# Optimization experiments

Hardware: AMD Instinct MI355X
Metric: run time of the kernel (lower is better)

The kernel has to match this reference:

```python
import jax, jax.numpy as jnp
import numpy as np

NUM_LEVELS = 16
FEATS_PER_LEVEL = 2
LOG2_HASHMAP = 19
TABLE_SIZE = 1 << LOG2_HASHMAP
BASE_RES = 16
DESIRED_RES = 4096
PER_LEVEL_SCALE = float(np.exp(np.log(DESIRED_RES / BASE_RES) / (NUM_LEVELS - 1)))
PRIMES = (np.uint32(1), np.uint32(2654435761), np.uint32(805459861))
N_POINTS = 2_000_000


def _level_features(x, table, level):
    # x: [N,3] in [0,1]; table: [TABLE_SIZE, F]
    scale = BASE_RES * (PER_LEVEL_SCALE ** level) - 1.0
    res = int(np.ceil(scale)) + 1
    dense = (res ** 3) <= TABLE_SIZE  # tcnn uses dense indexing when grid fits
    pos = x * scale + 0.5
    pos0 = jnp.floor(pos)
    w = pos - pos0                     # trilinear weights, [N,3]
    base = pos0.astype(jnp.uint32)
    out = jnp.zeros((x.shape[0], table.shape[1]), dtype=table.dtype)
    for c in range(8):                 # 8 corners of the voxel
        offs = [(c >> d) & 1 for d in range(3)]
        pc = [jnp.minimum(base[:, d] + np.uint32(offs[d]), np.uint32(res - 1)) for d in range(3)]
        if dense:
            idx = pc[0] + pc[1] * np.uint32(res) + pc[2] * np.uint32(res * res)
        else:
            idx = (pc[0] * PRIMES[0]) ^ (pc[1] * PRIMES[1]) ^ (pc[2] * PRIMES[2])
            idx = idx & np.uint32(TABLE_SIZE - 1)
        wt = jnp.ones(x.shape[0], dtype=x.dtype)
        for d in range(3):
            wt = wt * (w[:, d] if offs[d] else (1.0 - w[:, d]))
        out = out + wt[:, None] * table[idx.astype(jnp.int32)]
    return out


def hashgrid_encode(x, tables):
    # x: [N,3] in [0,1]; tables: [L, TABLE_SIZE, F] -> [N, L*F]
    return jnp.concatenate(
        [_level_features(x, tables[l], l) for l in range(NUM_LEVELS)], axis=-1)


def setup_inputs() -> dict:
    key = jax.random.key(0)
    k1, k2, k3, k4, k5 = jax.random.split(key, 5)
    points = jax.random.uniform(k1, (N_POINTS, 3), dtype=jnp.float32)
    # tcnn hashgrid init: uniform(-1e-4, 1e-4)
    tables = jax.random.uniform(k2, (NUM_LEVELS, TABLE_SIZE, FEATS_PER_LEVEL),
                                minval=-1e-4, maxval=1e-4, dtype=jnp.float32)
    def kaiming(k, fan_out, fan_in):
        bound = np.sqrt(2.0) * np.sqrt(3.0 / fan_in)
        return jax.random.uniform(k, (fan_out, fan_in), minval=-bound, maxval=bound,
                                  dtype=jnp.float32)
    W1 = kaiming(k3, 32, 32)
    W2 = kaiming(k4, 32, 32)
    W3 = kaiming(k5, 4, 32)
    aabb = jnp.stack([jnp.zeros(3, jnp.float32), jnp.ones(3, jnp.float32)])
    return {"points": points, "tables": tables, "W1": W1, "W2": W2, "W3": W3,
            "aabb": aabb}


def reference(points, tables, W1, W2, W3, aabb):
    texc = jnp.clip((points - aabb[0][None, :]) / (aabb[1] - aabb[0])[None, :], 0.0, 1.0)
    enc = hashgrid_encode(texc, tables)            # [N, 32]
    h = jax.nn.relu(enc @ W1.T)
    h = jax.nn.relu(h @ W2.T)
    out = h @ W3.T                                 # [N, 4]
    mn = jnp.array([0.0, 0.0, 0.0, 0.01], dtype=out.dtype)
    mx = jnp.array([1.0, 1.0, 1.0, 1.0], dtype=out.dtype)
    return jax.nn.sigmoid(out) * (mx - mn) + mn
```

## Files before the change

### kernel.cpp

```cpp
#include <hip/hip_runtime.h>
#include <cmath>


namespace {
constexpr int kLevels = 16;
constexpr unsigned kTableSize = 1u << 19;
constexpr unsigned kMask = kTableSize - 1u;
constexpr int kCells = 262144;
constexpr int kScanBlocks = 256;

typedef _Float16 half2_t __attribute__((ext_vector_type(2)));
typedef unsigned int u32;

struct LevelParams {
  float scale[kLevels];
  unsigned res[kLevels];
  int dense[kLevels];
  unsigned toff[kLevels];
  unsigned cnt[kLevels];
};
}

__global__ __launch_bounds__(256)
void conv_tables_kernel(const float2* __restrict__ src, u32* __restrict__ dst,
                        LevelParams lp,
                        const float* __restrict__ W1, const float* __restrict__ W2,
                        const float* __restrict__ W3, half2_t* __restrict__ Wh,
                        u32* __restrict__ hist0)
{
  int gid = blockIdx.x * blockDim.x + threadIdx.x;
  if (gid < 512) {
    Wh[gid] = half2_t{(_Float16)W1[2 * gid], (_Float16)W1[2 * gid + 1]};
  } else if (gid < 1024) {
    int t = gid - 512;
    Wh[512 + t] = half2_t{(_Float16)W2[2 * t], (_Float16)W2[2 * t + 1]};
  } else if (gid < 1088) {
    int t = gid - 1024;
    Wh[1024 + t] = half2_t{(_Float16)W3[2 * t], (_Float16)W3[2 * t + 1]};
  }
  if (hist0 && gid < kCells) hist0[gid] = 0u;
  int l = blockIdx.x >> 11;
  unsigned e = (unsigned)((blockIdx.x & 2047) * blockDim.x + threadIdx.x);
  if (l < kLevels && e < lp.cnt[l]) {
    float2 v = src[(size_t)l * kTableSize + e];
    dst[lp.toff[l] + e] =
        __builtin_bit_cast(u32, half2_t{(_Float16)v.x, (_Float16)v.y});
  }
}

__device__ __forceinline__ void texc_of(const float* __restrict__ pts,
                                        const float* __restrict__ aabb, int i,
                                        float& x, float& y, float& z)
{
  float a0x = aabb[0], a0y = aabb[1], a0z = aabb[2];
  float a1x = aabb[3], a1y = aabb[4], a1z = aabb[5];
  x = fminf(fmaxf((pts[3 * i + 0] - a0x) / (a1x - a0x), 0.f), 1.f);
  y = fminf(fmaxf((pts[3 * i + 1] - a0y) / (a1y - a0y), 0.f), 1.f);
  z = fminf(fmaxf((pts[3 * i + 2] - a0z) / (a1z - a0z), 0.f), 1.f);
}

__device__ __forceinline__ u32 expand3(u32 v)
{
  v &= 0x3FFu;
  v = (v | (v << 16)) & 0x030000FFu;
  v = (v | (v << 8))  & 0x0300F00Fu;
  v = (v | (v << 4))  & 0x030C30C3u;
  v = (v | (v << 2))  & 0x09249249u;
  return v;
}

__device__ __forceinline__ u32 cell_of(float x, float y, float z)
{
  u32 cx = (u32)min((int)(x * 64.f), 63);
  u32 cy = (u32)min((int)(y * 64.f), 63);
  u32 cz = (u32)min((int)(z * 64.f), 63);
  return expand3(cx) | (expand3(cy) << 1) | (expand3(cz) << 2);
}

__global__ __launch_bounds__(256)
void hist_kernel(const float* __restrict__ points, const float* __restrict__ aabb,
                 u32* __restrict__ hist, int n)
{
  int i = blockIdx.x * blockDim.x + threadIdx.x;
  if (i >= n) return;
  float x, y, z;
  texc_of(points, aabb, i, x, y, z);
  atomicAdd(&hist[cell_of(x, y, z)], 1u);
}

__global__ __launch_bounds__(1024)
void scanA_kernel(u32* __restrict__ hist, u32* __restrict__ btot)
{
  __shared__ u32 sm[1024];
  int t = threadIdx.x;
  int i = (blockIdx.x << 10) + t;
  u32 x = hist[i];
  sm[t] = x;
  __syncthreads();
  u32 v = x;
  for (int off = 1; off < 1024; off <<= 1) {
    u32 a = (t >= off) ? sm[t - off] : 0u;
    __syncthreads();
    v += a;
    sm[t] = v;
    __syncthreads();
  }
  hist[i] = v - x;
  if (t == 1023) btot[blockIdx.x] = v;
}

__global__ __launch_bounds__(256)
void scatter_kernel(const float* __restrict__ points, const float* __restrict__ aabb,
                    u32* __restrict__ hist, const u32* __restrict__ btot,
                    float4* __restrict__ sorted, int n)
{
  __shared__ u32 bb[kScanBlocks];
  int t = threadIdx.x;
  u32 xv = btot[t];
  bb[t] = xv;
  __syncthreads();
  u32 v = xv;
  for (int off = 1; off < 256; off <<= 1) {
    u32 a = (t >= off) ? bb[t - off] : 0u;
    __syncthreads();
    v += a;
    bb[t] = v;
    __syncthreads();
  }
  u32 excl = v - xv;
  __syncthreads();
  bb[t] = excl;
  __syncthreads();

  int i = blockIdx.x * 256 + t;
  if (i >= n) return;
  float x, y, z;
  texc_of(points, aabb, i, x, y, z);
  u32 c = cell_of(x, y, z);
  u32 slot = bb[c >> 10] + atomicAdd(&hist[c], 1u);
  sorted[slot] = float4{x, y, z, __builtin_bit_cast(float, (u32)i)};
}

__device__ __forceinline__ u32 sel4(uint4 v, u32 j) {
  u32 lo = (j & 1u) ? v.y : v.x;
  u32 hi = (j & 1u) ? v.w : v.z;
  return (j & 2u) ? hi : lo;
}

__device__ __forceinline__ float dot2_acc(half2_t a, half2_t b, float c) {
#if __has_builtin(__builtin_amdgcn_fdot2)
  return __builtin_amdgcn_fdot2(a, b, c, false);
#else
  return c + (float)a.x * (float)b.x + (float)a.y * (float)b.y;
#endif
}

__global__ __launch_bounds__(256)
void encode_kernel(const float4* __restrict__ pts,
                   const u32* __restrict__ tables,
                   half2_t* __restrict__ enc,
                   LevelParams lp, int n, int bpl)
{
  int l = blockIdx.x / bpl;
  int i = (blockIdx.x - l * bpl) * blockDim.x + threadIdx.x;
  if (i >= n) return;

  float4 p = pts[i];
  float x = p.x, y = p.y, z = p.z;

  float s = lp.scale[l];
  unsigned res = lp.res[l];
  bool dense = (lp.dense[l] != 0);
  unsigned rm1 = res - 1u;
  unsigned res2 = res * res;
  const u32* tab = tables + lp.toff[l];

  float fx = x * s + 0.5f, fy = y * s + 0.5f, fz = z * s + 0.5f;
  float fx0 = floorf(fx), fy0 = floorf(fy), fz0 = floorf(fz);
  float wx = fx - fx0, wy = fy - fy0, wz = fz - fz0;
  unsigned bx = (unsigned)fx0, by = (unsigned)fy0, bz = (unsigned)fz0;

  unsigned pcx0 = min(bx, rm1), pcx1 = min(bx + 1u, rm1);

  u32 idx0[4], idx1[4];
  #pragma unroll
  for (int q = 0; q < 4; ++q) {
    unsigned oy = (unsigned)(q & 1);
    unsigned oz = (unsigned)(q >> 1);
    unsigned pcy = min(by + oy, rm1);
    unsigned pcz = min(bz + oz, rm1);
    if (dense) {
      u32 b = pcy * res + pcz * res2;
      idx0[q] = pcx0 + b;
      idx1[q] = pcx1 + b;
    } else {
      u32 h = (pcy * 2654435761u) ^ (pcz * 805459861u);
      idx0[q] = (pcx0 ^ h) & kMask;
      idx1[q] = (pcx1 ^ h) & kMask;
    }
  }

  uint4 v[4];
  #pragma unroll
  for (int q = 0; q < 4; ++q)
    v[q] = *reinterpret_cast<const uint4*>(tab + (idx0[q] & ~3u));

  u32 e1x[4] = {0u, 0u, 0u, 0u};
  #pragma unroll
  for (int q = 0; q < 4; ++q) {
    if ((idx0[q] ^ idx1[q]) >= 4u) e1x[q] = tab[idx1[q]];
  }

  float wx1 = wx, wx0 = 1.f - wx;
  float acc0 = 0.f, acc1 = 0.f;
  #pragma unroll
  for (int q = 0; q < 4; ++q) {
    unsigned oy = (unsigned)(q & 1);
    unsigned oz = (unsigned)(q >> 1);
    float wyz = (oy ? wy : 1.f - wy) * (oz ? wz : 1.f - wz);
    u32 e0 = sel4(v[q], idx0[q] & 3u);
    u32 e1g = sel4(v[q], idx1[q] & 3u);
    u32 e1 = ((idx0[q] ^ idx1[q]) < 4u) ? e1g : e1x[q];
    half2_t f0 = __builtin_bit_cast(half2_t, e0);
    half2_t f1 = __builtin_bit_cast(half2_t, e1);
    float w0 = wyz * wx0, w1 = wyz * wx1;
    acc0 += w0 * (float)f0.x + w1 * (float)f1.x;
    acc1 += w0 * (float)f0.y + w1 * (float)f1.y;
  }
  enc[(size_t)l * n + i] = half2_t{(_Float16)acc0, (_Float16)acc1};
}

__global__ __launch_bounds__(256)
void encode_raw_kernel(const float* __restrict__ points,
                       const u32* __restrict__ tables,
                       const float* __restrict__ aabb,
                       half2_t* __restrict__ enc,
                       LevelParams lp, int n, int bpl)
{
  int l = blockIdx.x / bpl;
  int i = (blockIdx.x - l * bpl) * blockDim.x + threadIdx.x;
  if (i >= n) return;
  float x, y, z;
  texc_of(points, aabb, i, x, y, z);

  float s = lp.scale[l];
  unsigned res = lp.res[l];
  bool dense = (lp.dense[l] != 0);
  unsigned rm1 = res - 1u;
  unsigned res2 = res * res;
  const u32* tab = tables + lp.toff[l];

  float fx = x * s + 0.5f, fy = y * s + 0.5f, fz = z * s + 0.5f;
  float fx0 = floorf(fx), fy0 = floorf(fy), fz0 = floorf(fz);
  float wx = fx - fx0, wy = fy - fy0, wz = fz - fz0;
  unsigned bx = (unsigned)fx0, by = (unsigned)fy0, bz = (unsigned)fz0;
  unsigned pcx0 = min(bx, rm1), pcx1 = min(bx + 1u, rm1);

  u32 idx0[4], idx1[4];
  #pragma unroll
  for (int q = 0; q < 4; ++q) {
    unsigned oy = (unsigned)(q & 1);
    unsigned oz = (unsigned)(q >> 1);
    unsigned pcy = min(by + oy, rm1);
    unsigned pcz = min(bz + oz, rm1);
    if (dense) {
      u32 b = pcy * res + pcz * res2;
      idx0[q] = pcx0 + b;
      idx1[q] = pcx1 + b;
    } else {
      u32 h = (pcy * 2654435761u) ^ (pcz * 805459861u);
      idx0[q] = (pcx0 ^ h) & kMask;
      idx1[q] = (pcx1 ^ h) & kMask;
    }
  }
  uint4 v[4];
  #pragma unroll
  for (int q = 0; q < 4; ++q)
    v[q] = *reinterpret_cast<const uint4*>(tab + (idx0[q] & ~3u));
  u32 e1x[4] = {0u, 0u, 0u, 0u};
  #pragma unroll
  for (int q = 0; q < 4; ++q) {
    if ((idx0[q] ^ idx1[q]) >= 4u) e1x[q] = tab[idx1[q]];
  }
  float wx1 = wx, wx0 = 1.f - wx;
  float acc0 = 0.f, acc1 = 0.f;
  #pragma unroll
  for (int q = 0; q < 4; ++q) {
    unsigned oy = (unsigned)(q & 1);
    unsigned oz = (unsigned)(q >> 1);
    float wyz = (oy ? wy : 1.f - wy) * (oz ? wz : 1.f - wz);
    u32 e0 = sel4(v[q], idx0[q] & 3u);
    u32 e1g = sel4(v[q], idx1[q] & 3u);
    u32 e1 = ((idx0[q] ^ idx1[q]) < 4u) ? e1g : e1x[q];
    half2_t f0 = __builtin_bit_cast(half2_t, e0);
    half2_t f1 = __builtin_bit_cast(half2_t, e1);
    float w0 = wyz * wx0, w1 = wyz * wx1;
    acc0 += w0 * (float)f0.x + w1 * (float)f1.x;
    acc1 += w0 * (float)f0.y + w1 * (float)f1.y;
  }
  enc[(size_t)l * n + i] = half2_t{(_Float16)acc0, (_Float16)acc1};
}

__global__ __launch_bounds__(256)
void mlp_kernel(const half2_t* __restrict__ enc,
                const half2_t* __restrict__ Wh,
                const float* __restrict__ sortedw,
                float* __restrict__ out, int n)
{
  int i = blockIdx.x * blockDim.x + threadIdx.x;
  if (i >= n) return;

  u32 orig = sortedw ? __builtin_bit_cast(u32, sortedw[4 * i + 3]) : (u32)i;

  half2_t e[16];
  #pragma unroll
  for (int l = 0; l < kLevels; ++l) e[l] = enc[(size_t)l * n + i];

  const half2_t* W1h = Wh;
  const half2_t* W2h = Wh + 512;
  const half2_t* W3h = Wh + 1024;

  half2_t h1[16];
  #pragma unroll
  for (int jj = 0; jj < 16; ++jj) {
    float a0 = 0.f, a1 = 0.f;
    #pragma unroll
    for (int k = 0; k < 16; ++k) {
      a0 = dot2_acc(e[k], W1h[16 * (2 * jj) + k], a0);
      a1 = dot2_acc(e[k], W1h[16 * (2 * jj + 1) + k], a1);
    }
    h1[jj] = half2_t{(_Float16)fmaxf(a0, 0.f), (_Float16)fmaxf(a1, 0.f)};
  }

  half2_t h2[16];
  #pragma unroll
  for (int jj = 0; jj < 16; ++jj) {
    float a0 = 0.f, a1 = 0.f;
    #pragma unroll
    for (int k = 0; k < 16; ++k) {
      a0 = dot2_acc(h1[k], W2h[16 * (2 * jj) + k], a0);
      a1 = dot2_acc(h1[k], W2h[16 * (2 * jj + 1) + k], a1);
    }
    h2[jj] = half2_t{(_Float16)fmaxf(a0, 0.f), (_Float16)fmaxf(a1, 0.f)};
  }

  float o[4];
  #pragma unroll
  for (int j = 0; j < 4; ++j) {
    float acc = 0.f;
    #pragma unroll
    for (int k = 0; k < 16; ++k) acc = dot2_acc(h2[k], W3h[16 * j + k], acc);
    o[j] = acc;
  }

  float4 r;
  r.x = 1.f / (1.f + __expf(-o[0]));
  r.y = 1.f / (1.f + __expf(-o[1]));
  r.z = 1.f / (1.f + __expf(-o[2]));
  r.w = 0.99f / (1.f + __expf(-o[3])) + 0.01f;
  reinterpret_cast<float4*>(out)[orig] = r;
}

__global__ __launch_bounds__(256)
void hashgrid_mlp_kernel(const float* __restrict__ points,
                         const float* __restrict__ tables,
                         const float* __restrict__ W1,
                         const float* __restrict__ W2,
                         const float* __restrict__ W3,
                         const float* __restrict__ aabb,
                         float* __restrict__ out,
                         LevelParams lp, int n)
{
  int i = blockIdx.x * blockDim.x + threadIdx.x;
  if (i >= n) return;
  float x, y, z;
  texc_of(points, aabb, i, x, y, z);
  float enc[2 * kLevels];
  #pragma unroll
  for (int l = 0; l < kLevels; ++l) {
    float s = lp.scale[l];
    unsigned res = lp.res[l];
    bool dense = (lp.dense[l] != 0);
    unsigned rm1 = res - 1u;
    unsigned res2 = res * res;
    float fx = x * s + 0.5f, fy = y * s + 0.5f, fz = z * s + 0.5f;
    float fx0 = floorf(fx), fy0 = floorf(fy), fz0 = floorf(fz);
    float wx = fx - fx0, wy = fy - fy0, wz = fz - fz0;
    unsigned bx = (unsigned)fx0, by = (unsigned)fy0, bz = (unsigned)fz0;
    const float2* tab = reinterpret_cast<const float2*>(tables) + (size_t)l * kTableSize;
    float acc0 = 0.f, acc1 = 0.f;
    #pragma unroll
    for (int c = 0; c < 8; ++c) {
      unsigned ox = (unsigned)(c & 1);
      unsigned oy = (unsigned)((c >> 1) & 1);
      unsigned oz = (unsigned)((c >> 2) & 1);
      unsigned pcx = min(bx + ox, rm1);
      unsigned pcy = min(by + oy, rm1);
      unsigned pcz = min(bz + oz, rm1);
      unsigned idx;
      if (dense) idx = pcx + pcy * res + pcz * res2;
      else idx = (pcx ^ (pcy * 2654435761u) ^ (pcz * 805459861u)) & kMask;
      float wt = (ox ? wx : 1.f - wx) * (oy ? wy : 1.f - wy) * (oz ? wz : 1.f - wz);
      float2 f = tab[idx];
      acc0 += wt * f.x;
      acc1 += wt * f.y;
    }
    enc[2 * l + 0] = acc0;
    enc[2 * l + 1] = acc1;
  }
  float h1[32];
  #pragma unroll
  for (int j = 0; j < 32; ++j) {
    float acc = 0.f;
    #pragma unroll
    for (int k = 0; k < 32; ++k) acc += enc[k] * W1[32 * j + k];
    h1[j] = fmaxf(acc, 0.f);
  }
  float h2[32];
  #pragma unroll
  for (int j = 0; j < 32; ++j) {
    float acc = 0.f;
    #pragma unroll
    for (int k = 0; k < 32; ++k) acc += h1[k] * W2[32 * j + k];
    h2[j] = fmaxf(acc, 0.f);
  }
  float o[4];
  #pragma unroll
  for (int j = 0; j < 4; ++j) {
    float acc = 0.f;
    #pragma unroll
    for (int k = 0; k < 32; ++k) acc += h2[k] * W3[32 * j + k];
    o[j] = acc;
  }
  float4 r;
  r.x = 1.f / (1.f + __expf(-o[0]));
  r.y = 1.f / (1.f + __expf(-o[1]));
  r.z = 1.f / (1.f + __expf(-o[2]));
  r.w = 0.99f / (1.f + __expf(-o[3])) + 0.01f;
  reinterpret_cast<float4*>(out)[i] = r;
}

extern "C" void kernel_launch(void* const* d_in, const int* in_sizes, int n_in,
                              void* d_out, int out_size, void* d_ws, size_t ws_size,
                              hipStream_t stream) {
  const float* points = (const float*)d_in[0];
  const float* tables = (const float*)d_in[1];
  const float* W1     = (const float*)d_in[2];
  const float* W2     = (const float*)d_in[3];
  const float* W3     = (const float*)d_in[4];
  const float* aabb   = (const float*)d_in[5];
  float* out = (float*)d_out;
  int n = in_sizes[0] / 3;

  LevelParams lp;
  const double pls = std::exp(std::log(4096.0 / 16.0) / 15.0);
  unsigned off = 0;
  for (int l = 0; l < kLevels; ++l) {
    double s = 16.0 * std::pow(pls, (double)l) - 1.0;
    lp.scale[l] = (float)s;
    long long res = (long long)std::ceil(s) + 1;
    lp.res[l] = (unsigned)res;
    long long r3 = res * res * res;
    lp.dense[l] = (r3 <= (long long)kTableSize) ? 1 : 0;
    lp.cnt[l] = lp.dense[l] ? (unsigned)r3 : kTableSize;
    lp.toff[l] = off;
    off += (lp.cnt[l] + 3u) & ~3u;
  }

  const int block = 256;
  const size_t tab_f16_bytes = (size_t)off * sizeof(u32);
  const size_t sorted_bytes  = (size_t)n * sizeof(float4);
  const size_t hist_bytes    = (size_t)(kCells + kScanBlocks) * sizeof(u32);
  const size_t enc_bytes     = (size_t)kLevels * (size_t)n * sizeof(half2_t);
  const size_t w_bytes       = 1088 * sizeof(half2_t);

  const size_t need_sorted = tab_f16_bytes + sorted_bytes + hist_bytes +
                             enc_bytes + w_bytes;
  const size_t need_sorted_real = tab_f16_bytes + sorted_bytes + enc_bytes + w_bytes;
  const size_t need_sorted_tight = tab_f16_bytes + enc_bytes + w_bytes +
                                   ((size_t)n * sizeof(u32));
  (void)need_sorted_tight;

  const size_t need_raw = tab_f16_bytes + enc_bytes + w_bytes;
  const bool out_fits_scratch = (size_t)out_size >= (size_t)4 * (size_t)n;

  const int grid_n = (n + block - 1) / block;
  const int bpl = grid_n;

  if (ws_size >= need_sorted_real) {
    char* p = (char*)d_ws;
    u32*     tab_f16 = (u32*)p;                   p += tab_f16_bytes;
    float4*  sorted  = (float4*)p;                p += sorted_bytes;
    half2_t* enc     = (half2_t*)p;               p += enc_bytes;
    half2_t* Wh      = (half2_t*)p;
    u32*     hist    = (u32*)enc;
    u32*     btot    = hist + kCells;

    conv_tables_kernel<<<kLevels * 2048, block, 0, stream>>>(
        reinterpret_cast<const float2*>(tables), tab_f16, lp, W1, W2, W3, Wh, hist);
    hist_kernel<<<grid_n, block, 0, stream>>>(points, aabb, hist, n);
    scanA_kernel<<<kScanBlocks, 1024, 0, stream>>>(hist, btot);
    scatter_kernel<<<grid_n, block, 0, stream>>>(points, aabb, hist, btot,
                                                 sorted, n);
    encode_kernel<<<bpl * kLevels, block, 0, stream>>>(
        sorted, tab_f16, enc, lp, n, bpl);
    mlp_kernel<<<grid_n, block, 0, stream>>>(enc, Wh, (const float*)sorted, out, n);
  } else if (ws_size >= need_raw && out_fits_scratch) {
    char* p = (char*)d_ws;
    u32*     tab_f16 = (u32*)p;                   p += tab_f16_bytes;
    half2_t* enc     = (half2_t*)p;               p += enc_bytes;
    half2_t* Wh      = (half2_t*)p;
    u32*     hist    = (u32*)enc;
    u32*     btot    = hist + kCells;
    float4*  sorted  = (float4*)d_out;

    conv_tables_kernel<<<kLevels * 2048, block, 0, stream>>>(
        reinterpret_cast<const float2*>(tables), tab_f16, lp, W1, W2, W3, Wh, hist);
    hist_kernel<<<grid_n, block, 0, stream>>>(points, aabb, hist, n);
    scanA_kernel<<<kScanBlocks, 1024, 0, stream>>>(hist, btot);
    scatter_kernel<<<grid_n, block, 0, stream>>>(points, aabb, hist, btot,
                                                 sorted, n);
    encode_kernel<<<bpl * kLevels, block, 0, stream>>>(
        sorted, tab_f16, enc, lp, n, bpl);
    mlp_kernel<<<grid_n, block, 0, stream>>>(enc, Wh, (const float*)sorted, out, n);
  } else if (ws_size >= need_raw) {
    char* p = (char*)d_ws;
    u32*     tab_f16 = (u32*)p;                   p += tab_f16_bytes;
    half2_t* enc     = (half2_t*)p;               p += enc_bytes;
    half2_t* Wh      = (half2_t*)p;

    conv_tables_kernel<<<kLevels * 2048, block, 0, stream>>>(
        reinterpret_cast<const float2*>(tables), tab_f16, lp, W1, W2, W3, Wh,
        nullptr);
    encode_raw_kernel<<<bpl * kLevels, block, 0, stream>>>(
        points, tab_f16, aabb, enc, lp, n, bpl);
    mlp_kernel<<<grid_n, block, 0, stream>>>(enc, Wh, nullptr, out, n);
  } else {
    hashgrid_mlp_kernel<<<grid_n, block, 0, stream>>>(
        points, tables, W1, W2, W3, aabb, out, lp, n);
  }
}
```

Before: 821.2 us.

## Use row-major cell sort, separate perm array, per-level encode launches

Replaces the Morton-order cell key with a simple linear x/y/z cell index and stores the original point index in a separate perm array instead of the float4's w lane. The sorted points buffer moves into the output buffer. Encoding is split into one kernel that loops over all dense levels per point, plus one launch per hashed level. The per-level launches are meant to keep each hash table's working set hot in cache, at the cost of more kernel launches and a different spatial ordering.

New measurement: 843.6 us. 2.7% more time.

```diff
diff --git a/kernel.cpp b/kernel.cpp
--- a/kernel.cpp
+++ b/kernel.cpp
@@ -59,22 +59,12 @@
   z = fminf(fmaxf((pts[3 * i + 2] - a0z) / (a1z - a0z), 0.f), 1.f);
 }
 
-__device__ __forceinline__ u32 expand3(u32 v)
-{
-  v &= 0x3FFu;
-  v = (v | (v << 16)) & 0x030000FFu;
-  v = (v | (v << 8))  & 0x0300F00Fu;
-  v = (v | (v << 4))  & 0x030C30C3u;
-  v = (v | (v << 2))  & 0x09249249u;
-  return v;
-}
-
 __device__ __forceinline__ u32 cell_of(float x, float y, float z)
 {
-  u32 cx = (u32)min((int)(x * 64.f), 63);
-  u32 cy = (u32)min((int)(y * 64.f), 63);
-  u32 cz = (u32)min((int)(z * 64.f), 63);
-  return expand3(cx) | (expand3(cy) << 1) | (expand3(cz) << 2);
+  int cx = min((int)(x * 64.f), 63);
+  int cy = min((int)(y * 64.f), 63);
+  int cz = min((int)(z * 64.f), 63);
+  return (u32)(cx + (cy << 6) + (cz << 12));
 }
 
 __global__ __launch_bounds__(256)
@@ -112,7 +102,7 @@
 __global__ __launch_bounds__(256)
 void scatter_kernel(const float* __restrict__ points, const float* __restrict__ aabb,
                     u32* __restrict__ hist, const u32* __restrict__ btot,
-                    float4* __restrict__ sorted, int n)
+                    float4* __restrict__ sorted, u32* __restrict__ perm, int n)
 {
   __shared__ u32 bb[kScanBlocks];
   int t = threadIdx.x;
@@ -138,7 +128,8 @@
   texc_of(points, aabb, i, x, y, z);
   u32 c = cell_of(x, y, z);
   u32 slot = bb[c >> 10] + atomicAdd(&hist[c], 1u);
-  sorted[slot] = float4{x, y, z, __builtin_bit_cast(float, (u32)i)};
+  sorted[slot] = float4{x, y, z, 0.f};
+  perm[slot] = (u32)i;
 }
 
 __device__ __forceinline__ u32 sel4(uint4 v, u32 j) {
@@ -155,31 +146,16 @@
 #endif
 }
 
-__global__ __launch_bounds__(256)
-void encode_kernel(const float4* __restrict__ pts,
-                   const u32* __restrict__ tables,
-                   half2_t* __restrict__ enc,
-                   LevelParams lp, int n, int bpl)
-{
-  int l = blockIdx.x / bpl;
-  int i = (blockIdx.x - l * bpl) * blockDim.x + threadIdx.x;
-  if (i >= n) return;
-
-  float4 p = pts[i];
-  float x = p.x, y = p.y, z = p.z;
-
-  float s = lp.scale[l];
-  unsigned res = lp.res[l];
-  bool dense = (lp.dense[l] != 0);
+__device__ __forceinline__ u32 encode_level(float x, float y, float z,
+                                            float s, unsigned res, bool dense,
+                                            const u32* __restrict__ tab)
+{
   unsigned rm1 = res - 1u;
   unsigned res2 = res * res;
-  const u32* tab = tables + lp.toff[l];
-
   float fx = x * s + 0.5f, fy = y * s + 0.5f, fz = z * s + 0.5f;
   float fx0 = floorf(fx), fy0 = floorf(fy), fz0 = floorf(fz);
   float wx = fx - fx0, wy = fy - fy0, wz = fz - fz0;
   unsigned bx = (unsigned)fx0, by = (unsigned)fy0, bz = (unsigned)fz0;
-
   unsigned pcx0 = min(bx, rm1), pcx1 = min(bx + 1u, rm1);
 
   u32 idx0[4], idx1[4];
@@ -199,18 +175,15 @@
       idx1[q] = (pcx1 ^ h) & kMask;
     }
   }
-
   uint4 v[4];
   #pragma unroll
   for (int q = 0; q < 4; ++q)
     v[q] = *reinterpret_cast<const uint4*>(tab + (idx0[q] & ~3u));
-
   u32 e1x[4] = {0u, 0u, 0u, 0u};
   #pragma unroll
   for (int q = 0; q < 4; ++q) {
     if ((idx0[q] ^ idx1[q]) >= 4u) e1x[q] = tab[idx1[q]];
   }
-
   float wx1 = wx, wx0 = 1.f - wx;
   float acc0 = 0.f, acc1 = 0.f;
   #pragma unroll
@@ -227,14 +200,43 @@
     acc0 += w0 * (float)f0.x + w1 * (float)f1.x;
     acc1 += w0 * (float)f0.y + w1 * (float)f1.y;
   }
-  enc[(size_t)l * n + i] = half2_t{(_Float16)acc0, (_Float16)acc1};
+  return __builtin_bit_cast(u32, half2_t{(_Float16)acc0, (_Float16)acc1});
+}
+
+__global__ __launch_bounds__(256)
+void encode_dense_kernel(const float4* __restrict__ pts,
+                         const u32* __restrict__ tables,
+                         u32* __restrict__ enc,
+                         LevelParams lp, int nd, int n)
+{
+  int i = blockIdx.x * blockDim.x + threadIdx.x;
+  if (i >= n) return;
+  float4 p = pts[i];
+  #pragma unroll 1
+  for (int l = 0; l < nd; ++l) {
+    enc[(size_t)l * n + i] = encode_level(p.x, p.y, p.z, lp.scale[l], lp.res[l],
+                                          lp.dense[l] != 0, tables + lp.toff[l]);
+  }
+}
+
+__global__ __launch_bounds__(256)
+void encode_level_kernel(const float4* __restrict__ pts,
+                         const u32* __restrict__ tables,
+                         u32* __restrict__ enc,
+                         LevelParams lp, int l, int n)
+{
+  int i = blockIdx.x * blockDim.x + threadIdx.x;
+  if (i >= n) return;
+  float4 p = pts[i];
+  enc[(size_t)l * n + i] = encode_level(p.x, p.y, p.z, lp.scale[l], lp.res[l],
+                                        lp.dense[l] != 0, tables + lp.toff[l]);
 }
 
 __global__ __launch_bounds__(256)
 void encode_raw_kernel(const float* __restrict__ points,
                        const u32* __restrict__ tables,
                        const float* __restrict__ aabb,
-                       half2_t* __restrict__ enc,
+                       u32* __restrict__ enc,
                        LevelParams lp, int n, int bpl)
 {
   int l = blockIdx.x / bpl;
@@ -242,79 +244,25 @@
   if (i >= n) return;
   float x, y, z;
   texc_of(points, aabb, i, x, y, z);
-
-  float s = lp.scale[l];
-  unsigned res = lp.res[l];
-  bool dense = (lp.dense[l] != 0);
-  unsigned rm1 = res - 1u;
-  unsigned res2 = res * res;
-  const u32* tab = tables + lp.toff[l];
-
-  float fx = x * s + 0.5f, fy = y * s + 0.5f, fz = z * s + 0.5f;
-  float fx0 = floorf(fx), fy0 = floorf(fy), fz0 = floorf(fz);
-  float wx = fx - fx0, wy = fy - fy0, wz = fz - fz0;
-  unsigned bx = (unsigned)fx0, by = (unsigned)fy0, bz = (unsigned)fz0;
-  unsigned pcx0 = min(bx, rm1), pcx1 = min(bx + 1u, rm1);
-
-  u32 idx0[4], idx1[4];
-  #pragma unroll
-  for (int q = 0; q < 4; ++q) {
-    unsigned oy = (unsigned)(q & 1);
-    unsigned oz = (unsigned)(q >> 1);
-    unsigned pcy = min(by + oy, rm1);
-    unsigned pcz = min(bz + oz, rm1);
-    if (dense) {
-      u32 b = pcy * res + pcz * res2;
-      idx0[q] = pcx0 + b;
-      idx1[q] = pcx1 + b;
-    } else {
-      u32 h = (pcy * 2654435761u) ^ (pcz * 805459861u);
-      idx0[q] = (pcx0 ^ h) & kMask;
-      idx1[q] = (pcx1 ^ h) & kMask;
-    }
-  }
-  uint4 v[4];
-  #pragma unroll
-  for (int q = 0; q < 4; ++q)
-    v[q] = *reinterpret_cast<const uint4*>(tab + (idx0[q] & ~3u));
-  u32 e1x[4] = {0u, 0u, 0u, 0u};
-  #pragma unroll
-  for (int q = 0; q < 4; ++q) {
-    if ((idx0[q] ^ idx1[q]) >= 4u) e1x[q] = tab[idx1[q]];
-  }
-  float wx1 = wx, wx0 = 1.f - wx;
-  float acc0 = 0.f, acc1 = 0.f;
-  #pragma unroll
-  for (int q = 0; q < 4; ++q) {
-    unsigned oy = (unsigned)(q & 1);
-    unsigned oz = (unsigned)(q >> 1);
-    float wyz = (oy ? wy : 1.f - wy) * (oz ? wz : 1.f - wz);
-    u32 e0 = sel4(v[q], idx0[q] & 3u);
-    u32 e1g = sel4(v[q], idx1[q] & 3u);
-    u32 e1 = ((idx0[q] ^ idx1[q]) < 4u) ? e1g : e1x[q];
-    half2_t f0 = __builtin_bit_cast(half2_t, e0);
-    half2_t f1 = __builtin_bit_cast(half2_t, e1);
-    float w0 = wyz * wx0, w1 = wyz * wx1;
-    acc0 += w0 * (float)f0.x + w1 * (float)f1.x;
-    acc1 += w0 * (float)f0.y + w1 * (float)f1.y;
-  }
-  enc[(size_t)l * n + i] = half2_t{(_Float16)acc0, (_Float16)acc1};
-}
-
-__global__ __launch_bounds__(256)
-void mlp_kernel(const half2_t* __restrict__ enc,
+  enc[(size_t)l * n + i] = encode_level(x, y, z, lp.scale[l], lp.res[l],
+                                        lp.dense[l] != 0, tables + lp.toff[l]);
+}
+
+__global__ __launch_bounds__(256)
+void mlp_kernel(const u32* __restrict__ enc,
                 const half2_t* __restrict__ Wh,
-                const float* __restrict__ sortedw,
+                const u32* __restrict__ perm,
                 float* __restrict__ out, int n)
 {
   int i = blockIdx.x * blockDim.x + threadIdx.x;
   if (i >= n) return;
 
-  u32 orig = sortedw ? __builtin_bit_cast(u32, sortedw[4 * i + 3]) : (u32)i;
+  u32 orig = perm ? perm[i] : (u32)i;
 
   half2_t e[16];
   #pragma unroll
-  for (int l = 0; l < kLevels; ++l) e[l] = enc[(size_t)l * n + i];
+  for (int l = 0; l < kLevels; ++l)
+    e[l] = __builtin_bit_cast(half2_t, enc[(size_t)l * n + i]);
 
   const half2_t* W1h = Wh;
   const half2_t* W2h = Wh + 512;
@@ -455,6 +403,7 @@
   LevelParams lp;
   const double pls = std::exp(std::log(4096.0 / 16.0) / 15.0);
   unsigned off = 0;
+  int ndense = 0;
   for (int l = 0; l < kLevels; ++l) {
     double s = 16.0 * std::pow(pls, (double)l) - 1.0;
     lp.scale[l] = (float)s;
@@ -466,69 +415,51 @@
     lp.toff[l] = off;
     off += (lp.cnt[l] + 3u) & ~3u;
   }
+  for (int l = 0; l < kLevels; ++l) { if (lp.dense[l]) ndense = l + 1; else break; }
 
   const int block = 256;
   const size_t tab_f16_bytes = (size_t)off * sizeof(u32);
-  const size_t sorted_bytes  = (size_t)n * sizeof(float4);
-  const size_t hist_bytes    = (size_t)(kCells + kScanBlocks) * sizeof(u32);
-  const size_t enc_bytes     = (size_t)kLevels * (size_t)n * sizeof(half2_t);
+  const size_t enc_bytes     = (size_t)kLevels * (size_t)n * sizeof(u32);
+  const size_t perm_bytes    = (size_t)n * sizeof(u32);
   const size_t w_bytes       = 1088 * sizeof(half2_t);
 
-  const size_t need_sorted = tab_f16_bytes + sorted_bytes + hist_bytes +
-                             enc_bytes + w_bytes;
-  const size_t need_sorted_real = tab_f16_bytes + sorted_bytes + enc_bytes + w_bytes;
-  const size_t need_sorted_tight = tab_f16_bytes + enc_bytes + w_bytes +
-                                   ((size_t)n * sizeof(u32));
-  (void)need_sorted_tight;
-
-  const size_t need_raw = tab_f16_bytes + enc_bytes + w_bytes;
+  const size_t need_sorted = tab_f16_bytes + enc_bytes + perm_bytes + w_bytes;
+  const size_t need_raw    = tab_f16_bytes + enc_bytes + w_bytes;
   const bool out_fits_scratch = (size_t)out_size >= (size_t)4 * (size_t)n;
+  const bool enc_fits_hist = enc_bytes >= (size_t)(kCells + kScanBlocks) * sizeof(u32);
 
   const int grid_n = (n + block - 1) / block;
-  const int bpl = grid_n;
-
-  if (ws_size >= need_sorted_real) {
+
+  if (ws_size >= need_sorted && out_fits_scratch && enc_fits_hist) {
     char* p = (char*)d_ws;
     u32*     tab_f16 = (u32*)p;                   p += tab_f16_bytes;
-    float4*  sorted  = (float4*)p;                p += sorted_bytes;
-    half2_t* enc     = (half2_t*)p;               p += enc_bytes;
+    u32*     enc     = (u32*)p;                   p += enc_bytes;
+    u32*     perm    = (u32*)p;                   p += perm_bytes;
     half2_t* Wh      = (half2_t*)p;
-    u32*     hist    = (u32*)enc;
+    u32*     hist    = enc;
     u32*     btot    = hist + kCells;
+    float4*  sorted  = (float4*)d_out;
 
     conv_tables_kernel<<<kLevels * 2048, block, 0, stream>>>(
         reinterpret_cast<const float2*>(tables), tab_f16, lp, W1, W2, W3, Wh, hist);
     hist_kernel<<<grid_n, block, 0, stream>>>(points, aabb, hist, n);
     scanA_kernel<<<kScanBlocks, 1024, 0, stream>>>(hist, btot);
     scatter_kernel<<<grid_n, block, 0, stream>>>(points, aabb, hist, btot,
-                                                 sorted, n);
-    encode_kernel<<<bpl * kLevels, block, 0, stream>>>(
-        sorted, tab_f16, enc, lp, n, bpl);
-    mlp_kernel<<<grid_n, block, 0, stream>>>(enc, Wh, (const float*)sorted, out, n);
-  } else if (ws_size >= need_raw && out_fits_scratch) {
-    char* p = (char*)d_ws;
-    u32*     tab_f16 = (u32*)p;                   p += tab_f16_bytes;
-    half2_t* enc     = (half2_t*)p;               p += enc_bytes;
-    half2_t* Wh      = (half2_t*)p;
-    u32*     hist    = (u32*)enc;
-    u32*     btot    = hist + kCells;
-    float4*  sorted  = (float4*)d_out;
-
-    conv_tables_kernel<<<kLevels * 2048, block, 0, stream>>>(
-        reinterpret_cast<const float2*>(tables), tab_f16, lp, W1, W2, W3, Wh, hist);
-    hist_kernel<<<grid_n, block, 0, stream>>>(points, aabb, hist, n);
-    scanA_kernel<<<kScanBlocks, 1024, 0, stream>>>(hist, btot);
-    scatter_kernel<<<grid_n, block, 0, stream>>>(points, aabb, hist, btot,
-                                                 sorted, n);
-    encode_kernel<<<bpl * kLevels, block, 0, stream>>>(
-        sorted, tab_f16, enc, lp, n, bpl);
-    mlp_kernel<<<grid_n, block, 0, stream>>>(enc, Wh, (const float*)sorted, out, n);
+                                                 sorted, perm, n);
+    encode_dense_kernel<<<grid_n, block, 0, stream>>>(sorted, tab_f16, enc,
+                                                      lp, ndense, n);
+    for (int l = ndense; l < kLevels; ++l) {
+      encode_level_kernel<<<grid_n, block, 0, stream>>>(sorted, tab_f16, enc,
+                                                        lp, l, n);
+    }
+    mlp_kernel<<<grid_n, block, 0, stream>>>(enc, Wh, perm, out, n);
   } else if (ws_size >= need_raw) {
     char* p = (char*)d_ws;
     u32*     tab_f16 = (u32*)p;                   p += tab_f16_bytes;
-    half2_t* enc     = (half2_t*)p;               p += enc_bytes;
+    u32*     enc     = (u32*)p;                   p += enc_bytes;
     half2_t* Wh      = (half2_t*)p;
 
+    const int bpl = grid_n;
     conv_tables_kernel<<<kLevels * 2048, block, 0, stream>>>(
         reinterpret_cast<const float2*>(tables), tab_f16, lp, W1, W2, W3, Wh,
         nullptr);
```
